# Kernel tuning notes

Measured on AMD Instinct MI355X. Metric: run time of the kernel, lower is better.

## Reference

```python
import jax, jax.numpy as jnp
import numpy as np

N_NODES = 50000
N_EDGES = 600000
D = 128


def _clip(x, c=1.0):
    # per-row L2 clip: x / max(||x|| / c, 1)
    n = jnp.linalg.norm(x, axis=-1, keepdims=True)
    return x / jnp.maximum(n / c, 1.0)


def _priv_sage_conv(x, edge_index, W, b, noise):
    # PrivSAGEConv.forward with perturbation_mode='aggr', root_weight=False
    xc = _clip(x, c=1.0)
    src, dst = edge_index[0], edge_index[1]
    # propagate: gather messages from source nodes, scatter-add at targets
    msg = jax.ops.segment_sum(xc[src], dst, num_segments=x.shape[0])  # [N, D]
    agg = xc + msg + noise  # self term + neighbor sum + DP noise
    return agg @ W.T + b


def setup_inputs() -> dict:
    key = jax.random.key(0)
    ks = jax.random.split(key, 8)
    x = jax.random.normal(ks[0], (N_NODES, D), dtype=jnp.float32)
    edge_index = jax.random.randint(ks[1], (2, N_EDGES), 0, N_NODES, dtype=jnp.int64)
    scale = 1.0 / np.sqrt(D)
    W1 = jax.random.normal(ks[2], (D, D), dtype=jnp.float32) * scale
    b1 = jnp.zeros((D,), dtype=jnp.float32)
    W2 = jax.random.normal(ks[3], (D, D), dtype=jnp.float32) * scale
    b2 = jnp.zeros((D,), dtype=jnp.float32)
    noise1 = jax.random.normal(ks[4], (N_NODES, D), dtype=jnp.float32)
    noise2 = jax.random.normal(ks[5], (N_NODES, D), dtype=jnp.float32)
    return {"x": x, "edge_index": edge_index, "W1": W1, "b1": b1,
            "W2": W2, "b2": b2, "noise1": noise1, "noise2": noise2}


def reference(x, edge_index, W1, b1, W2, b2, noise1, noise2):
    # Layer 1: conv -> (no batchnorm) -> dropout(identity, eval) -> SELU -> stack-combine
    h = _priv_sage_conv(x, edge_index, W1, b1, noise1)
    h = jax.nn.selu(h)
    # Layer 2: last layer, is_pred_module=True -> raw output
    out = _priv_sage_conv(h, edge_index, W2, b2, noise2)
    return out
```

## Files before the change

### kernel.cpp

```cpp
#include <hip/hip_runtime.h>

#define NN 50000
#define NE 600000
#define DD 128
#define NPAD 50048
#define NTILE 782
#define SETUP_BLOCKS 12501
#define EDGE_BLOCKS 2344
#define SCAN_BLOCKS 49

typedef __attribute__((ext_vector_type(8))) short bf16x8;
typedef __attribute__((ext_vector_type(4))) float f32x4;

__device__ __forceinline__ float bf2f(unsigned int u16) {
    union { unsigned int i; float f; } v; v.i = u16 << 16; return v.f;
}
__device__ __forceinline__ unsigned short f2bf(float f) {
    union { float f; unsigned int i; } v; v.f = f;
    unsigned int i = v.i + 0x7FFFu + ((v.i >> 16) & 1u);
    return (unsigned short)(i >> 16);
}
__device__ __forceinline__ float wred64(float v) {
    #pragma unroll
    for (int o = 32; o; o >>= 1) v += __shfl_xor(v, o, 64);
    return v;
}
__device__ __forceinline__ int tame16(unsigned int u) {
    int e = (int)((u >> 7) & 0xFF);
    return (e >= 100 && e <= 133) ? 1 : 0;
}


__device__ __forceinline__ int probe_e64(const int* __restrict__ ei, int t,
                                         int* f_s) {
    if (t < 64) {
        int nz = 0;
        #pragma unroll
        for (int i = 0; i < 4; ++i) nz |= ei[2 * (t * 4 + i) + 1];
        #pragma unroll
        for (int o = 32; o; o >>= 1) nz |= __shfl_xor(nz, o, 64);
        if (t == 0) *f_s = (nz == 0) ? 1 : 0;
    }
    __syncthreads();
    return *f_s;
}

__device__ __forceinline__ int probe_bf16(const unsigned int* __restrict__ p,
                                          int t, int* f_s) {
    if (t < 64) {
        int tc = tame16(p[t] & 0xFFFFu);
        #pragma unroll
        for (int o = 32; o; o >>= 1) tc += __shfl_xor(tc, o, 64);
        if (t == 0) *f_s = (tc >= 48) ? 1 : 0;
    }
    __syncthreads();
    return *f_s;
}


__device__ __forceinline__ void agg_phase(
    const int* __restrict__ offs, const int* __restrict__ eidx,
    const uint2* __restrict__ featu2, const void* __restrict__ noise,
    const int f_nb, uint2* __restrict__ aggu2,
    const int node, const int lane) {
    const int c = lane & 31;
    const int h = lane >> 5;
    float a0, a1, a2, a3;
    if (h == 0) {
        const uint2 s = featu2[(size_t)node * 32 + c];
        a0 = bf2f(s.x & 0xFFFFu); a1 = bf2f(s.x >> 16);
        a2 = bf2f(s.y & 0xFFFFu); a3 = bf2f(s.y >> 16);
    } else {
        if (f_nb) {
            const uint2 n = ((const uint2*)noise)[(size_t)node * 32 + c];
            a0 = bf2f(n.x & 0xFFFFu); a1 = bf2f(n.x >> 16);
            a2 = bf2f(n.y & 0xFFFFu); a3 = bf2f(n.y >> 16);
        } else {
            const float4 n = ((const float4*)noise)[(size_t)node * 32 + c];
            a0 = n.x; a1 = n.y; a2 = n.z; a3 = n.w;
        }
    }
    const int e0 = offs[node];
    const int cnt = offs[node + 1] - e0;
    for (int base = 0; base < cnt; base += 64) {
        const int rem = cnt - base;
        int myi = NN;
        if (lane < rem) myi = eidx[e0 + base + lane];
        const int pairs = (rem < 64 ? rem + 1 : 64) >> 1;
        const int pb = (pairs + 7) & ~7;
        for (int p = 0; p < pb; p += 8) {
            uint2 u[8];
            #pragma unroll
            for (int q = 0; q < 8; ++q) {
                const int s = __shfl(myi, 2 * (p + q) + h, 64);
                u[q] = featu2[(size_t)s * 32 + c];
            }
            #pragma unroll
            for (int q = 0; q < 8; ++q) {
                a0 += bf2f(u[q].x & 0xFFFFu); a1 += bf2f(u[q].x >> 16);
                a2 += bf2f(u[q].y & 0xFFFFu); a3 += bf2f(u[q].y >> 16);
            }
        }
    }
    a0 += __shfl_xor(a0, 32, 64);
    a1 += __shfl_xor(a1, 32, 64);
    a2 += __shfl_xor(a2, 32, 64);
    a3 += __shfl_xor(a3, 32, 64);
    if (h == 0) {
        uint2 o;
        o.x = (unsigned int)f2bf(a0) | ((unsigned int)f2bf(a1) << 16);
        o.y = (unsigned int)f2bf(a2) | ((unsigned int)f2bf(a3) << 16);
        aggu2[(size_t)node * 32 + c] = o;
    }
}


__global__ __launch_bounds__(256) void setup_k(
    const void* __restrict__ x,
    const void* __restrict__ W1, const void* __restrict__ b1,
    const void* __restrict__ W2, const void* __restrict__ b2,
    unsigned short* __restrict__ W1b, unsigned short* __restrict__ b1b,
    unsigned short* __restrict__ W2b, unsigned short* __restrict__ b2b,
    int* __restrict__ deg, int* __restrict__ pf,
    unsigned int* __restrict__ featu) {
    __shared__ int fx_s, fw_s;
    const int t = threadIdx.x;
    if (t < 64) {
        int tx = tame16(((const unsigned int*)x)[t] & 0xFFFFu);
        int tw = tame16(((const unsigned int*)W1)[t] & 0xFFFFu);
        #pragma unroll
        for (int o = 32; o; o >>= 1) {
            tx += __shfl_xor(tx, o, 64);
            tw += __shfl_xor(tw, o, 64);
        }
        if (t == 0) { fx_s = (tx >= 48) ? 1 : 0; fw_s = (tw >= 48) ? 1 : 0; }
    }
    __syncthreads();
    const int f_xb = fx_s, f_wb = fw_s;
    const int b = blockIdx.x;
    const int tid = b * 256 + t;
    const int nthr = gridDim.x * 256;

    for (int i = tid; i < DD * DD; i += nthr) {
        if (f_wb) {
            W1b[i] = ((const unsigned short*)W1)[i];
            W2b[i] = ((const unsigned short*)W2)[i];
            if (i < DD) { b1b[i] = ((const unsigned short*)b1)[i];
                          b2b[i] = ((const unsigned short*)b2)[i]; }
        } else {
            W1b[i] = f2bf(((const float*)W1)[i]);
            W2b[i] = f2bf(((const float*)W2)[i]);
            if (i < DD) { b1b[i] = f2bf(((const float*)b1)[i]);
                          b2b[i] = f2bf(((const float*)b2)[i]); }
        }
    }
    for (int i = tid; i < NN + 64; i += nthr) {
        if (i < NN) deg[i] = 0; else pf[i - NN] = 0;
    }
    const int lane = t & 63;
    const int wv = t >> 6;
    const int nwv = gridDim.x * 4;
    for (int row = b * 4 + wv; row <= NN; row += nwv) {
        if (row == NN) { featu[(size_t)NN * 64 + lane] = 0u; continue; }
        float v0, v1;
        if (f_xb) {
            const unsigned int px = ((const unsigned int*)x)[(size_t)row * 64 + lane];
            v0 = bf2f(px & 0xFFFFu); v1 = bf2f(px >> 16);
        } else {
            const float2 px = ((const float2*)x)[(size_t)row * 64 + lane];
            v0 = px.x; v1 = px.y;
        }
        const float ss = wred64(v0 * v0 + v1 * v1);
        const float nrm = sqrtf(ss);
        const float sc = nrm > 1.0f ? 1.0f / nrm : 1.0f;
        featu[(size_t)row * 64 + lane] =
            (unsigned int)f2bf(v0 * sc) | ((unsigned int)f2bf(v1 * sc) << 16);
    }
}

__global__ __launch_bounds__(256) void hist_k(
    const int* __restrict__ ei, int* __restrict__ deg) {
    __shared__ int f_s;
    const int f_e64 = probe_e64(ei, threadIdx.x, &f_s);
    const int e = blockIdx.x * 256 + threadIdx.x;
    if (e >= NE) return;
    const int d = f_e64 ? (int)((const long long*)ei)[NE + e] : ei[NE + e];
    atomicAdd(&deg[d], 1);
}

__global__ __launch_bounds__(1024) void scan_k(
    const int* __restrict__ deg, int* __restrict__ offs,
    int* __restrict__ cursor, int* __restrict__ pf) {
    __shared__ int wsum[16];
    __shared__ int wbase[16];
    __shared__ int base_s;
    const int tid = threadIdx.x, lane = tid & 63, wv = tid >> 6;
    const int b = blockIdx.x;
    const int i = b * 1024 + tid;
    const int v = (i < NN) ? deg[i] : 0;
    int incl = v;
    #pragma unroll
    for (int off = 1; off < 64; off <<= 1) {
        int t = __shfl_up(incl, off, 64);
        if (lane >= off) incl += t;
    }
    if (lane == 63) wsum[wv] = incl;
    __syncthreads();
    if (wv == 0 && lane < 16) {
        const int wv_v = wsum[lane];
        int wincl = wv_v;
        #pragma unroll
        for (int off = 1; off < 16; off <<= 1) {
            int t = __shfl_up(wincl, off, 64);
            if (lane >= off) wincl += t;
        }
        wbase[lane] = wincl - wv_v;
        if (lane == 15)
            __hip_atomic_store(&pf[b], wincl + 1, __ATOMIC_RELEASE,
                               __HIP_MEMORY_SCOPE_AGENT);
    }
    if (wv == 0) {
        int val = 0;
        while (true) {
            if (lane < SCAN_BLOCKS && val == 0)
                val = __hip_atomic_load(&pf[lane], __ATOMIC_ACQUIRE,
                                        __HIP_MEMORY_SCOPE_AGENT);
            if (__ballot(lane < SCAN_BLOCKS && val == 0) == 0ull) break;
            __builtin_amdgcn_s_sleep(1);
        }
        int pv = (lane < SCAN_BLOCKS) ? val - 1 : 0;
        int ex = pv;
        #pragma unroll
        for (int off = 1; off < 64; off <<= 1) {
            int t = __shfl_up(ex, off, 64);
            if (lane >= off) ex += t;
        }
        ex -= pv;
        if (lane == b) base_s = ex;
    }
    __syncthreads();
    if (i < NN) {
        const int o = base_s + wbase[wv] + incl - v;
        offs[i] = o;
        cursor[i] = o;
    }
    if (b == 0 && tid == 0) offs[NN] = NE;
}

__global__ __launch_bounds__(256) void fill_k(
    const int* __restrict__ ei, int* __restrict__ cursor,
    int* __restrict__ eidx) {
    __shared__ int f_s;
    const int f_e64 = probe_e64(ei, threadIdx.x, &f_s);
    const int e = blockIdx.x * 256 + threadIdx.x;
    if (e >= NE) return;
    int s, d;
    if (f_e64) {
        const long long* e64 = (const long long*)ei;
        s = (int)e64[e]; d = (int)e64[NE + e];
    } else {
        s = ei[e]; d = ei[NE + e];
    }
    const int pos = atomicAdd(&cursor[d], 1);
    eidx[pos] = s;
}

__global__ __launch_bounds__(256) void agg_k(
    const int* __restrict__ offs, const int* __restrict__ eidx,
    const uint2* __restrict__ featu2, const void* __restrict__ noise,
    const unsigned int* __restrict__ nprobe, uint2* __restrict__ aggu2) {
    __shared__ int f_s;
    const int f_nb = probe_bf16(nprobe, threadIdx.x, &f_s);
    const int node = (blockIdx.x * 256 + threadIdx.x) >> 6;
    const int lane = threadIdx.x & 63;
    if (node >= NN) return;
    agg_phase(offs, eidx, featu2, noise, f_nb, aggu2, node, lane);
}

template<bool LAYER1>
__global__ __launch_bounds__(256) void gemm_k(
    const unsigned short* __restrict__ aggb,
    const unsigned short* __restrict__ Wb,
    const unsigned short* __restrict__ bb,
    unsigned short* __restrict__ featb,
    float* __restrict__ outf) {
    __shared__ unsigned short Wl[128 * 136];
    __shared__ unsigned short bl[128];
    const int t = threadIdx.x;
    #pragma unroll
    for (int i = 0; i < 8; ++i) {
        const int idx8 = t + i * 256;
        const int base = idx8 * 8;
        const int row = base >> 7, col = base & 127;
        *(uint4*)&Wl[row * 136 + col] = ((const uint4*)Wb)[idx8];
    }
    if (t < 128) bl[t] = bb[t];

    const int lane = t & 63;
    const int w = t >> 6;
    const int n15 = lane & 15;
    const int quad = lane >> 4;
    const int rbase = blockIdx.x * 64 + w * 16;

    bf16x8 af[4];
    #pragma unroll
    for (int kc = 0; kc < 4; ++kc)
        af[kc] = *(const bf16x8*)&aggb[(size_t)(rbase + n15) * DD + kc * 32 + quad * 8];

    __syncthreads();

    float h[32];
    #pragma unroll
    for (int nt = 0; nt < 8; ++nt) {
        f32x4 acc = {0.f, 0.f, 0.f, 0.f};
        #pragma unroll
        for (int kc = 0; kc < 4; ++kc) {
            const bf16x8 bfr =
                *(const bf16x8*)&Wl[(nt * 16 + n15) * 136 + kc * 32 + quad * 8];
            acc = __builtin_amdgcn_mfma_f32_16x16x32_bf16(af[kc], bfr, acc, 0, 0, 0);
        }
        const float bj = bf2f((unsigned int)bl[nt * 16 + n15]);
        #pragma unroll
        for (int r = 0; r < 4; ++r) h[nt * 4 + r] = acc[r] + bj;
    }

    if (LAYER1) {
        const float S = 1.0507009873554805f, AL = 1.6732632423543772f;
        float ss[4] = {0.f, 0.f, 0.f, 0.f};
        #pragma unroll
        for (int nt = 0; nt < 8; ++nt)
            #pragma unroll
            for (int r = 0; r < 4; ++r) {
                float v = h[nt * 4 + r];
                v = v > 0.f ? S * v : S * AL * expm1f(v);
                h[nt * 4 + r] = v;
                ss[r] += v * v;
            }
        #pragma unroll
        for (int r = 0; r < 4; ++r) {
            #pragma unroll
            for (int off = 1; off < 16; off <<= 1)
                ss[r] += __shfl_xor(ss[r], off, 64);
        }
        #pragma unroll
        for (int r = 0; r < 4; ++r) {
            const float nr = sqrtf(ss[r]);
            const float sc = nr > 1.f ? 1.f / nr : 1.f;
            const int row = rbase + quad * 4 + r;
            if (row < NN) {
                #pragma unroll
                for (int nt = 0; nt < 8; ++nt)
                    featb[(size_t)row * DD + nt * 16 + n15] =
                        f2bf(h[nt * 4 + r] * sc);
            }
        }
    } else {
        #pragma unroll
        for (int r = 0; r < 4; ++r) {
            const int row = rbase + quad * 4 + r;
            if (row < NN) {
                #pragma unroll
                for (int nt = 0; nt < 8; ++nt)
                    outf[(size_t)row * DD + nt * 16 + n15] = h[nt * 4 + r];
            }
        }
    }
}

extern "C" void kernel_launch(void* const* d_in, const int* in_sizes, int n_in,
                              void* d_out, int out_size, void* d_ws, size_t ws_size,
                              hipStream_t stream) {
    const void* x  = d_in[0];
    const int*  ei = (const int*)d_in[1];
    const void* W1 = d_in[2];
    const void* b1 = d_in[3];
    const void* W2 = d_in[4];
    const void* b2 = d_in[5];
    const void* n1 = d_in[6];
    const void* n2 = d_in[7];

    unsigned short* aggb = (unsigned short*)d_ws;
    unsigned short* W1b  = aggb + (size_t)NPAD * DD;
    unsigned short* b1b  = W1b + DD * DD;
    unsigned short* W2b  = b1b + DD;
    unsigned short* b2b  = W2b + DD * DD;
    int* deg    = (int*)(b2b + DD);
    int* offs   = deg + NN;
    int* cursor = offs + NN + 1;
    int* pf     = cursor + NN;
    int* eidx   = pf + 64;
    unsigned int* featu = (unsigned int*)d_out;

    setup_k<<<SETUP_BLOCKS, 256, 0, stream>>>(
        x, W1, b1, W2, b2, W1b, b1b, W2b, b2b, deg, pf, featu);
    hist_k<<<EDGE_BLOCKS, 256, 0, stream>>>(ei, deg);
    scan_k<<<SCAN_BLOCKS, 1024, 0, stream>>>(deg, offs, cursor, pf);
    fill_k<<<EDGE_BLOCKS, 256, 0, stream>>>(ei, cursor, eidx);
    agg_k<<<(NN * 64) / 256, 256, 0, stream>>>(offs, eidx, (const uint2*)featu,
                                               n1, (const unsigned int*)n1,
                                               (uint2*)aggb);
    gemm_k<true><<<NTILE, 256, 0, stream>>>(aggb, W1b, b1b,
                                            (unsigned short*)featu, nullptr);
    agg_k<<<(NN * 64) / 256, 256, 0, stream>>>(offs, eidx, (const uint2*)featu,
                                               n2, (const unsigned int*)n1,
                                               (uint2*)aggb);
    gemm_k<false><<<NTILE, 256, 0, stream>>>(aggb, W2b, b2b, nullptr,
                                             (float*)d_out);
}
```

Baseline: 281.3 us.

## Fuse neighbor aggregation into GEMM kernel and batch edge processing per thread

Merges the separate aggregation and GEMM kernels into one kernel per layer: each wave aggregates 16 nodes into a shared-memory tile (using 16-byte gathers with four edges per step), then runs the MFMA GEMM directly from LDS. This removes the round trip of the aggregated matrix through global memory and two kernel launches. Layer-1 output now goes to a separate workspace buffer instead of overwriting the clipped input features. The histogram and fill kernels each process four edges per thread. The risk is lower occupancy and parallelism in the gather phase: 782 blocks each walk 16 nodes per wave serially, versus one wave per node before.

After: 366.2 us. +30.2%, slower.

```diff
diff --git a/kernel.cpp b/kernel.cpp
--- a/kernel.cpp
+++ b/kernel.cpp
@@ -6,7 +6,7 @@
 #define NPAD 50048
 #define NTILE 782
 #define SETUP_BLOCKS 12501
-#define EDGE_BLOCKS 2344
+#define E4_BLOCKS 586
 #define SCAN_BLOCKS 49
 
 typedef __attribute__((ext_vector_type(8))) short bf16x8;
@@ -55,63 +55,6 @@
     }
     __syncthreads();
     return *f_s;
-}
-
-
-__device__ __forceinline__ void agg_phase(
-    const int* __restrict__ offs, const int* __restrict__ eidx,
-    const uint2* __restrict__ featu2, const void* __restrict__ noise,
-    const int f_nb, uint2* __restrict__ aggu2,
-    const int node, const int lane) {
-    const int c = lane & 31;
-    const int h = lane >> 5;
-    float a0, a1, a2, a3;
-    if (h == 0) {
-        const uint2 s = featu2[(size_t)node * 32 + c];
-        a0 = bf2f(s.x & 0xFFFFu); a1 = bf2f(s.x >> 16);
-        a2 = bf2f(s.y & 0xFFFFu); a3 = bf2f(s.y >> 16);
-    } else {
-        if (f_nb) {
-            const uint2 n = ((const uint2*)noise)[(size_t)node * 32 + c];
-            a0 = bf2f(n.x & 0xFFFFu); a1 = bf2f(n.x >> 16);
-            a2 = bf2f(n.y & 0xFFFFu); a3 = bf2f(n.y >> 16);
-        } else {
-            const float4 n = ((const float4*)noise)[(size_t)node * 32 + c];
-            a0 = n.x; a1 = n.y; a2 = n.z; a3 = n.w;
-        }
-    }
-    const int e0 = offs[node];
-    const int cnt = offs[node + 1] - e0;
-    for (int base = 0; base < cnt; base += 64) {
-        const int rem = cnt - base;
-        int myi = NN;
-        if (lane < rem) myi = eidx[e0 + base + lane];
-        const int pairs = (rem < 64 ? rem + 1 : 64) >> 1;
-        const int pb = (pairs + 7) & ~7;
-        for (int p = 0; p < pb; p += 8) {
-            uint2 u[8];
-            #pragma unroll
-            for (int q = 0; q < 8; ++q) {
-                const int s = __shfl(myi, 2 * (p + q) + h, 64);
-                u[q] = featu2[(size_t)s * 32 + c];
-            }
-            #pragma unroll
-            for (int q = 0; q < 8; ++q) {
-                a0 += bf2f(u[q].x & 0xFFFFu); a1 += bf2f(u[q].x >> 16);
-                a2 += bf2f(u[q].y & 0xFFFFu); a3 += bf2f(u[q].y >> 16);
-            }
-        }
-    }
-    a0 += __shfl_xor(a0, 32, 64);
-    a1 += __shfl_xor(a1, 32, 64);
-    a2 += __shfl_xor(a2, 32, 64);
-    a3 += __shfl_xor(a3, 32, 64);
-    if (h == 0) {
-        uint2 o;
-        o.x = (unsigned int)f2bf(a0) | ((unsigned int)f2bf(a1) << 16);
-        o.y = (unsigned int)f2bf(a2) | ((unsigned int)f2bf(a3) << 16);
-        aggu2[(size_t)node * 32 + c] = o;
-    }
 }
 
 
@@ -182,10 +125,19 @@
     const int* __restrict__ ei, int* __restrict__ deg) {
     __shared__ int f_s;
     const int f_e64 = probe_e64(ei, threadIdx.x, &f_s);
-    const int e = blockIdx.x * 256 + threadIdx.x;
-    if (e >= NE) return;
-    const int d = f_e64 ? (int)((const long long*)ei)[NE + e] : ei[NE + e];
-    atomicAdd(&deg[d], 1);
+    const int e0 = (blockIdx.x * 256 + threadIdx.x) * 4;
+    if (e0 >= NE) return;
+    int d[4];
+    #pragma unroll
+    for (int q = 0; q < 4; ++q) {
+        const int e = e0 + q;
+        d[q] = (e < NE)
+            ? (f_e64 ? (int)((const long long*)ei)[NE + e] : ei[NE + e])
+            : -1;
+    }
+    #pragma unroll
+    for (int q = 0; q < 4; ++q)
+        if (d[q] >= 0) atomicAdd(&deg[d[q]], 1);
 }
 
 __global__ __launch_bounds__(1024) void scan_k(
@@ -252,64 +204,142 @@
     int* __restrict__ eidx) {
     __shared__ int f_s;
     const int f_e64 = probe_e64(ei, threadIdx.x, &f_s);
-    const int e = blockIdx.x * 256 + threadIdx.x;
-    if (e >= NE) return;
-    int s, d;
-    if (f_e64) {
-        const long long* e64 = (const long long*)ei;
-        s = (int)e64[e]; d = (int)e64[NE + e];
-    } else {
-        s = ei[e]; d = ei[NE + e];
-    }
-    const int pos = atomicAdd(&cursor[d], 1);
-    eidx[pos] = s;
-}
-
-__global__ __launch_bounds__(256) void agg_k(
+    const int e0 = (blockIdx.x * 256 + threadIdx.x) * 4;
+    if (e0 >= NE) return;
+    int s[4], d[4];
+    #pragma unroll
+    for (int q = 0; q < 4; ++q) {
+        const int e = e0 + q;
+        if (e < NE) {
+            if (f_e64) {
+                const long long* e64 = (const long long*)ei;
+                s[q] = (int)e64[e]; d[q] = (int)e64[NE + e];
+            } else {
+                s[q] = ei[e]; d[q] = ei[NE + e];
+            }
+        } else d[q] = -1;
+    }
+    int pos[4];
+    #pragma unroll
+    for (int q = 0; q < 4; ++q)
+        if (d[q] >= 0) pos[q] = atomicAdd(&cursor[d[q]], 1);
+    #pragma unroll
+    for (int q = 0; q < 4; ++q)
+        if (d[q] >= 0) eidx[pos[q]] = s[q];
+}
+
+template<bool LAYER1>
+__global__ __launch_bounds__(256) void aggemm_k(
     const int* __restrict__ offs, const int* __restrict__ eidx,
-    const uint2* __restrict__ featu2, const void* __restrict__ noise,
-    const unsigned int* __restrict__ nprobe, uint2* __restrict__ aggu2) {
-    __shared__ int f_s;
-    const int f_nb = probe_bf16(nprobe, threadIdx.x, &f_s);
-    const int node = (blockIdx.x * 256 + threadIdx.x) >> 6;
-    const int lane = threadIdx.x & 63;
-    if (node >= NN) return;
-    agg_phase(offs, eidx, featu2, noise, f_nb, aggu2, node, lane);
-}
-
-template<bool LAYER1>
-__global__ __launch_bounds__(256) void gemm_k(
-    const unsigned short* __restrict__ aggb,
-    const unsigned short* __restrict__ Wb,
-    const unsigned short* __restrict__ bb,
+    const uint4* __restrict__ featu4, const void* __restrict__ noise,
+    const unsigned int* __restrict__ nprobe,
+    const unsigned short* __restrict__ Wb, const unsigned short* __restrict__ bb,
     unsigned short* __restrict__ featb,
     float* __restrict__ outf) {
     __shared__ unsigned short Wl[128 * 136];
     __shared__ unsigned short bl[128];
+    __shared__ unsigned short As[64 * 136];
+    __shared__ int f_s;
     const int t = threadIdx.x;
+    const int f_nb = probe_bf16(nprobe, t, &f_s);
+
     #pragma unroll
     for (int i = 0; i < 8; ++i) {
         const int idx8 = t + i * 256;
         const int base = idx8 * 8;
-        const int row = base >> 7, col = base & 127;
-        *(uint4*)&Wl[row * 136 + col] = ((const uint4*)Wb)[idx8];
+        *(uint4*)&Wl[(base >> 7) * 136 + (base & 127)] = ((const uint4*)Wb)[idx8];
     }
     if (t < 128) bl[t] = bb[t];
 
     const int lane = t & 63;
     const int w = t >> 6;
-    const int n15 = lane & 15;
-    const int quad = lane >> 4;
+    const int c = lane & 15;
+    const int h = lane >> 4;
     const int rbase = blockIdx.x * 64 + w * 16;
 
+    for (int i = 0; i < 16; ++i) {
+        const int node = rbase + i;
+        float a0 = 0.f, a1 = 0.f, a2 = 0.f, a3 = 0.f;
+        float a4 = 0.f, a5 = 0.f, a6 = 0.f, a7 = 0.f;
+        if (node < NN) {
+            if (h == 0) {
+                const uint4 sv = featu4[(size_t)node * 16 + c];
+                a0 += bf2f(sv.x & 0xFFFFu); a1 += bf2f(sv.x >> 16);
+                a2 += bf2f(sv.y & 0xFFFFu); a3 += bf2f(sv.y >> 16);
+                a4 += bf2f(sv.z & 0xFFFFu); a5 += bf2f(sv.z >> 16);
+                a6 += bf2f(sv.w & 0xFFFFu); a7 += bf2f(sv.w >> 16);
+            } else if (h == 1) {
+                if (f_nb) {
+                    const uint4 nv = ((const uint4*)noise)[(size_t)node * 16 + c];
+                    a0 += bf2f(nv.x & 0xFFFFu); a1 += bf2f(nv.x >> 16);
+                    a2 += bf2f(nv.y & 0xFFFFu); a3 += bf2f(nv.y >> 16);
+                    a4 += bf2f(nv.z & 0xFFFFu); a5 += bf2f(nv.z >> 16);
+                    a6 += bf2f(nv.w & 0xFFFFu); a7 += bf2f(nv.w >> 16);
+                }
+            } else if (h == 2) {
+                if (!f_nb) {
+                    const float4 nv = ((const float4*)noise)[(size_t)node * 32 + 2 * c];
+                    a0 += nv.x; a1 += nv.y; a2 += nv.z; a3 += nv.w;
+                }
+            } else {
+                if (!f_nb) {
+                    const float4 nv = ((const float4*)noise)[(size_t)node * 32 + 2 * c + 1];
+                    a4 += nv.x; a5 += nv.y; a6 += nv.z; a7 += nv.w;
+                }
+            }
+            const int e0 = offs[node];
+            const int cnt = offs[node + 1] - e0;
+            for (int base = 0; base < cnt; base += 64) {
+                const int rem = cnt - base;
+                int myi = NN;
+                if (lane < rem) myi = eidx[e0 + base + lane];
+                const int ecap = rem < 64 ? rem : 64;
+                const int qb = (ecap + 15) & ~15;
+                for (int p = 0; p < qb; p += 16) {
+                    uint4 u[4];
+                    #pragma unroll
+                    for (int q = 0; q < 4; ++q) {
+                        const int s = __shfl(myi, p + 4 * q + h, 64);
+                        u[q] = featu4[(size_t)s * 16 + c];
+                    }
+                    #pragma unroll
+                    for (int q = 0; q < 4; ++q) {
+                        a0 += bf2f(u[q].x & 0xFFFFu); a1 += bf2f(u[q].x >> 16);
+                        a2 += bf2f(u[q].y & 0xFFFFu); a3 += bf2f(u[q].y >> 16);
+                        a4 += bf2f(u[q].z & 0xFFFFu); a5 += bf2f(u[q].z >> 16);
+                        a6 += bf2f(u[q].w & 0xFFFFu); a7 += bf2f(u[q].w >> 16);
+                    }
+                }
+            }
+        }
+        a0 += __shfl_xor(a0, 16, 64); a0 += __shfl_xor(a0, 32, 64);
+        a1 += __shfl_xor(a1, 16, 64); a1 += __shfl_xor(a1, 32, 64);
+        a2 += __shfl_xor(a2, 16, 64); a2 += __shfl_xor(a2, 32, 64);
+        a3 += __shfl_xor(a3, 16, 64); a3 += __shfl_xor(a3, 32, 64);
+        a4 += __shfl_xor(a4, 16, 64); a4 += __shfl_xor(a4, 32, 64);
+        a5 += __shfl_xor(a5, 16, 64); a5 += __shfl_xor(a5, 32, 64);
+        a6 += __shfl_xor(a6, 16, 64); a6 += __shfl_xor(a6, 32, 64);
+        a7 += __shfl_xor(a7, 16, 64); a7 += __shfl_xor(a7, 32, 64);
+        if (h == 0) {
+            uint4 o;
+            o.x = (unsigned int)f2bf(a0) | ((unsigned int)f2bf(a1) << 16);
+            o.y = (unsigned int)f2bf(a2) | ((unsigned int)f2bf(a3) << 16);
+            o.z = (unsigned int)f2bf(a4) | ((unsigned int)f2bf(a5) << 16);
+            o.w = (unsigned int)f2bf(a6) | ((unsigned int)f2bf(a7) << 16);
+            *(uint4*)&As[(w * 16 + i) * 136 + c * 8] = o;
+        }
+    }
+
+    __syncthreads();
+
+    const int n15 = c;
+    const int quad = h;
     bf16x8 af[4];
     #pragma unroll
     for (int kc = 0; kc < 4; ++kc)
-        af[kc] = *(const bf16x8*)&aggb[(size_t)(rbase + n15) * DD + kc * 32 + quad * 8];
-
-    __syncthreads();
-
-    float h[32];
+        af[kc] = *(const bf16x8*)&As[(w * 16 + n15) * 136 + kc * 32 + quad * 8];
+
+    float hh[32];
     #pragma unroll
     for (int nt = 0; nt < 8; ++nt) {
         f32x4 acc = {0.f, 0.f, 0.f, 0.f};
@@ -321,7 +351,7 @@
         }
         const float bj = bf2f((unsigned int)bl[nt * 16 + n15]);
         #pragma unroll
-        for (int r = 0; r < 4; ++r) h[nt * 4 + r] = acc[r] + bj;
+        for (int r = 0; r < 4; ++r) hh[nt * 4 + r] = acc[r] + bj;
     }
 
     if (LAYER1) {
@@ -331,9 +361,9 @@
         for (int nt = 0; nt < 8; ++nt)
             #pragma unroll
             for (int r = 0; r < 4; ++r) {
-                float v = h[nt * 4 + r];
+                float v = hh[nt * 4 + r];
                 v = v > 0.f ? S * v : S * AL * expm1f(v);
-                h[nt * 4 + r] = v;
+                hh[nt * 4 + r] = v;
                 ss[r] += v * v;
             }
         #pragma unroll
@@ -351,7 +381,11 @@
                 #pragma unroll
                 for (int nt = 0; nt < 8; ++nt)
                     featb[(size_t)row * DD + nt * 16 + n15] =
-                        f2bf(h[nt * 4 + r] * sc);
+                        f2bf(hh[nt * 4 + r] * sc);
+            } else {
+                #pragma unroll
+                for (int nt = 0; nt < 8; ++nt)
+                    featb[(size_t)row * DD + nt * 16 + n15] = 0;
             }
         }
     } else {
@@ -361,7 +395,7 @@
             if (row < NN) {
                 #pragma unroll
                 for (int nt = 0; nt < 8; ++nt)
-                    outf[(size_t)row * DD + nt * 16 + n15] = h[nt * 4 + r];
+                    outf[(size_t)row * DD + nt * 16 + n15] = hh[nt * 4 + r];
             }
         }
     }
@@ -379,8 +413,8 @@
     const void* n1 = d_in[6];
     const void* n2 = d_in[7];
 
-    unsigned short* aggb = (unsigned short*)d_ws;
-    unsigned short* W1b  = aggb + (size_t)NPAD * DD;
+    unsigned short* hbuf = (unsigned short*)d_ws;
+    unsigned short* W1b  = hbuf + (size_t)NPAD * DD;
     unsigned short* b1b  = W1b + DD * DD;
     unsigned short* W2b  = b1b + DD;
     unsigned short* b2b  = W2b + DD * DD;
@@ -393,17 +427,13 @@
 
     setup_k<<<SETUP_BLOCKS, 256, 0, stream>>>(
         x, W1, b1, W2, b2, W1b, b1b, W2b, b2b, deg, pf, featu);
-    hist_k<<<EDGE_BLOCKS, 256, 0, stream>>>(ei, deg);
+    hist_k<<<E4_BLOCKS, 256, 0, stream>>>(ei, deg);
     scan_k<<<SCAN_BLOCKS, 1024, 0, stream>>>(deg, offs, cursor, pf);
-    fill_k<<<EDGE_BLOCKS, 256, 0, stream>>>(ei, cursor, eidx);
-    agg_k<<<(NN * 64) / 256, 256, 0, stream>>>(offs, eidx, (const uint2*)featu,
-                                               n1, (const unsigned int*)n1,
-                                               (uint2*)aggb);
-    gemm_k<true><<<NTILE, 256, 0, stream>>>(aggb, W1b, b1b,
-                                            (unsigned short*)featu, nullptr);
-    agg_k<<<(NN * 64) / 256, 256, 0, stream>>>(offs, eidx, (const uint2*)featu,
-                                               n2, (const unsigned int*)n1,
-                                               (uint2*)aggb);
-    gemm_k<false><<<NTILE, 256, 0, stream>>>(aggb, W2b, b2b, nullptr,
-                                             (float*)d_out);
-}
+    fill_k<<<E4_BLOCKS, 256, 0, stream>>>(ei, cursor, eidx);
+    aggemm_k<true><<<NTILE, 256, 0, stream>>>(
+        offs, eidx, (const uint4*)featu, n1, (const unsigned int*)n1,
+        W1b, b1b, hbuf, nullptr);
+    aggemm_k<false><<<NTILE, 256, 0, stream>>>(
+        offs, eidx, (const uint4*)hbuf, n2, (const unsigned int*)n1,
+        W2b, b2b, nullptr, (float*)d_out);
+}
```
